# Performance work log

Hardware: AMD Instinct MI355X
Metric: run time of the kernel (lower is better)

## Reference

```python
import jax, jax.numpy as jnp
import numpy as np

DIM = 1536
NH = 24
HD = DIM // NH
EPS = 1e-5


def _ln(x, gamma):
    # LayerNorm over last dim (head_dim), affine weight only, no bias
    mu = jnp.mean(x, axis=-1, keepdims=True)
    var = jnp.var(x, axis=-1, keepdims=True)
    return (x - mu) * jax.lax.rsqrt(var + EPS) * gamma


def setup_inputs() -> dict:
    key = jax.random.key(0)
    ks = jax.random.split(key, 24)
    B, S, T = 1, 2048, 512
    std = 0.02
    d = {
        "hidden_states": jax.random.normal(ks[0], (B, S, DIM), jnp.float32),
        "encoder_hidden_states": jax.random.normal(ks[1], (B, T, DIM), jnp.float32),
        "Wq": jax.random.normal(ks[2], (DIM, DIM), jnp.float32) * std,
        "bq": jnp.zeros((DIM,), jnp.float32),
        "Wk": jax.random.normal(ks[3], (DIM, DIM), jnp.float32) * std,
        "bk": jnp.zeros((DIM,), jnp.float32),
        "Wv": jax.random.normal(ks[4], (DIM, DIM), jnp.float32) * std,
        "bv": jnp.zeros((DIM,), jnp.float32),
        "Waq": jax.random.normal(ks[5], (DIM, DIM), jnp.float32) * std,
        "baq": jnp.zeros((DIM,), jnp.float32),
        "Wak": jax.random.normal(ks[6], (DIM, DIM), jnp.float32) * std,
        "bak": jnp.zeros((DIM,), jnp.float32),
        "Wav": jax.random.normal(ks[7], (DIM, DIM), jnp.float32) * std,
        "bav": jnp.zeros((DIM,), jnp.float32),
        "Wo": jax.random.normal(ks[8], (DIM, DIM), jnp.float32) * std,
        "bo": jnp.zeros((DIM,), jnp.float32),
        "Wao": jax.random.normal(ks[9], (DIM, DIM), jnp.float32) * std,
        "bao": jnp.zeros((DIM,), jnp.float32),
        "gq": jnp.ones((HD,), jnp.float32),
        "gk": jnp.ones((HD,), jnp.float32),
        "gaq": jnp.ones((HD,), jnp.float32),
        "gak": jnp.ones((HD,), jnp.float32),
    }
    return d


def reference(hidden_states, encoder_hidden_states, Wq, bq, Wk, bk, Wv, bv,
              Waq, baq, Wak, bak, Wav, bav, Wo, bo, Wao, bao, gq, gk, gaq, gak):
    B, S, _ = hidden_states.shape
    T = encoder_hidden_states.shape[1]

    def proj(x, W, b):
        # nn.Linear: x @ W.T + b ; reshape to (B, L, NH, HD)
        y = jnp.einsum('bld,ed->ble', x, W) + b
        return y.reshape(B, -1, NH, HD)

    q = _ln(proj(hidden_states, Wq, bq), gq)
    k = _ln(proj(hidden_states, Wk, bk), gk)
    v = proj(hidden_states, Wv, bv)
    eq = _ln(proj(encoder_hidden_states, Waq, baq), gaq)
    ek = _ln(proj(encoder_hidden_states, Wak, bak), gak)
    ev = proj(encoder_hidden_states, Wav, bav)

    q_cat = jnp.concatenate([q, eq], axis=1)  # (B, S+T, H, D)
    k_cat = jnp.concatenate([k, ek], axis=1)
    v_cat = jnp.concatenate([v, ev], axis=1)

    scale = 1.0 / np.sqrt(HD).astype(np.float32)
    scores = jnp.einsum('bqhd,bkhd->bhqk', q_cat, k_cat) * scale
    attn = jax.nn.softmax(scores, axis=-1)
    out = jnp.einsum('bhqk,bkhd->bqhd', attn, v_cat).reshape(B, S + T, DIM)

    img_out = jnp.einsum('bld,ed->ble', out[:, :S], Wo) + bo
    txt_out = jnp.einsum('bld,ed->ble', out[:, S:], Wao) + bao
    return (img_out, txt_out)
```

## Files before the change

### kernel.cpp

```cpp
#include <hip/hip_runtime.h>

#define DIMD 1536
#define LTOT 2560
#define NS 2048
#define NT 512

typedef __bf16 bf16x8 __attribute__((ext_vector_type(8)));
typedef float f32x4 __attribute__((ext_vector_type(4)));
typedef int i32x2 __attribute__((ext_vector_type(2)));
typedef unsigned short u16;
typedef unsigned int u32;

__device__ __forceinline__ u16 f2bf(float f) {
  union { float f; unsigned u; } v; v.f = f;
  return (u16)((v.u + 0x7fffu + ((v.u >> 16) & 1u)) >> 16);
}

__device__ __forceinline__ u32 cvt_pk_bf16(float a, float b) {
  u32 r;
  asm("v_cvt_pk_bf16_f32 %0, %1, %2" : "=v"(r) : "v"(a), "v"(b));
  return r;
}

__device__ __forceinline__ void gload_lds16(const void* g, void* l) {
  __builtin_amdgcn_global_load_lds(
      (__attribute__((address_space(1))) void*)(g),
      (__attribute__((address_space(3))) void*)(l), 16, 0, 0);
}

struct CvtArgs {
  const float* src[10];
  u16* dst[10];
  int n[10];
};

__global__ __launch_bounds__(256) void cvt_all(CvtArgs a) {
  const int seg = blockIdx.y;
  const int n = a.n[seg];
  const float* s = a.src[seg];
  u16* d = a.dst[seg];
  const int i = (blockIdx.x * 256 + threadIdx.x) * 4;
  if (i < n) {
    float4 v = *reinterpret_cast<const float4*>(s + i);
    ushort4 o;
    o.x = f2bf(v.x); o.y = f2bf(v.y); o.z = f2bf(v.z); o.w = f2bf(v.w);
    *reinterpret_cast<ushort4*>(d + i) = o;
  }
}

__device__ __forceinline__ void gemm_mainloop(
    const u16* __restrict__ A, const u16* __restrict__ W,
    u16* As, u16* Bs, f32x4 (&acc)[4][4],
    int w, int lane, int wr, int wc, int l15, int lh) {
  for (int k0 = 0; k0 < DIMD; k0 += 32) {
#pragma unroll
    for (int p = 0; p < 2; ++p) {
      const int c = p * 256 + w * 64 + lane;
      const int row = c >> 2, col = (c & 3) * 8;
      gload_lds16(A + (long)row * DIMD + k0 + col, As + (p * 256 + w * 64) * 8);
      gload_lds16(W + (long)row * DIMD + k0 + col, Bs + (p * 256 + w * 64) * 8);
    }
    __syncthreads();
    bf16x8 af[4], bfr[4];
#pragma unroll
    for (int m = 0; m < 4; ++m)
      af[m] = *reinterpret_cast<const bf16x8*>(As + (wr + m * 16 + l15) * 32 + lh * 8);
#pragma unroll
    for (int n = 0; n < 4; ++n)
      bfr[n] = *reinterpret_cast<const bf16x8*>(Bs + (wc + n * 16 + l15) * 32 + lh * 8);
#pragma unroll
    for (int m = 0; m < 4; ++m)
#pragma unroll
      for (int n = 0; n < 4; ++n)
        acc[m][n] = __builtin_amdgcn_mfma_f32_16x16x32_bf16(af[m], bfr[n], acc[m][n], 0, 0, 0);
    __syncthreads();
  }
}

struct QkvArgs {
  const u16* xb; const u16* exb;
  const u16* w[6];
  const float* b[6];
  const float* g[4];
  u16* qcat; u16* kcat; u16* vcat;
};

__global__ __launch_bounds__(256) void qkv_gemm(QkvArgs a) {
  __shared__ u16 As[128 * 32];
  __shared__ u16 Bs[128 * 32];
  const int tid = threadIdx.x, lane = tid & 63, w = tid >> 6;
  const int l15 = lane & 15, lh = lane >> 4;
  const int side = (blockIdx.x >= 16);
  const int mb = side ? (blockIdx.x - 16) : blockIdx.x;
  const int sel = blockIdx.y / 12;
  const int n0 = (blockIdx.y % 12) * 128;
  const long m0 = (long)mb * 128;
  const long Lbase = side ? NS : 0;
  const int wr = (w >> 1) * 64, wc = (w & 1) * 64;
  const u16* A = (side ? a.exb : a.xb) + m0 * DIMD;
  const u16* W = a.w[side * 3 + sel] + (long)n0 * DIMD;
  const float* bias = a.b[side * 3 + sel];

  f32x4 acc[4][4] = {};
  gemm_mainloop(A, W, As, Bs, acc, w, lane, wr, wc, l15, lh);

  if (sel == 2) {
    u16* out = a.vcat;
#pragma unroll
    for (int m = 0; m < 4; ++m)
#pragma unroll
      for (int r = 0; r < 4; ++r) {
        const long row = Lbase + m0 + wr + m * 16 + lh * 4 + r;
#pragma unroll
        for (int n = 0; n < 4; ++n)
          out[row * DIMD + n0 + wc + n * 16 + l15] =
              f2bf(acc[m][n][r] + bias[n0 + wc + n * 16 + l15]);
      }
  } else {
    const float* gamma = a.g[side * 2 + sel];
    const float gscale = (sel == 0) ? 0.125f * 1.4426950408889634f : 1.0f;
    u16* out = (sel == 0) ? a.qcat : a.kcat;
    const int swz = (sel == 1);
#pragma unroll
    for (int m = 0; m < 4; ++m) {
      float val[4][4];
#pragma unroll
      for (int n = 0; n < 4; ++n) {
        const float b = bias[n0 + wc + n * 16 + l15];
#pragma unroll
        for (int r = 0; r < 4; ++r) val[n][r] = acc[m][n][r] + b;
      }
      float s1[4], s2[4];
#pragma unroll
      for (int r = 0; r < 4; ++r) {
        s1[r] = 0.f; s2[r] = 0.f;
#pragma unroll
        for (int n = 0; n < 4; ++n) { s1[r] += val[n][r]; s2[r] += val[n][r] * val[n][r]; }
      }
#pragma unroll
      for (int off = 1; off < 16; off <<= 1) {
#pragma unroll
        for (int r = 0; r < 4; ++r) {
          s1[r] += __shfl_xor(s1[r], off, 16);
          s2[r] += __shfl_xor(s2[r], off, 16);
        }
      }
#pragma unroll
      for (int r = 0; r < 4; ++r) {
        const float mu = s1[r] * (1.0f / 64.0f);
        const float var = s2[r] * (1.0f / 64.0f) - mu * mu;
        const float rstd = rsqrtf(var + 1e-5f);
        const long row = Lbase + m0 + wr + m * 16 + lh * 4 + r;
        const int r7s = ((lh * 4 + r) & 7) << 3;
#pragma unroll
        for (int n = 0; n < 4; ++n) {
          const float g = gamma[n * 16 + l15] * gscale;
          const int colg = n0 + wc + n * 16 + l15;
          const int colstore = swz ? ((colg & ~63) | ((colg & 63) ^ r7s)) : colg;
          out[row * DIMD + colstore] = f2bf((val[n][r] - mu) * rstd * g);
        }
      }
    }
  }
}

struct OutArgs {
  const u16* aout;
  const u16* w[2];
  const float* b[2];
  float* out;
};

__global__ __launch_bounds__(256) void out_gemm(OutArgs a) {
  __shared__ u16 As[128 * 32];
  __shared__ u16 Bs[128 * 32];
  const int tid = threadIdx.x, lane = tid & 63, w = tid >> 6;
  const int l15 = lane & 15, lh = lane >> 4;
  const int side = (blockIdx.x >= 16);
  const int mb = side ? (blockIdx.x - 16) : blockIdx.x;
  const int n0 = blockIdx.y * 128;
  const long m0 = (long)mb * 128;
  const long Lbase = side ? NS : 0;
  const int wr = (w >> 1) * 64, wc = (w & 1) * 64;
  const u16* A = a.aout + (Lbase + m0) * DIMD;
  const u16* W = a.w[side] + (long)n0 * DIMD;
  const float* bias = a.b[side];

  f32x4 acc[4][4] = {};
  gemm_mainloop(A, W, As, Bs, acc, w, lane, wr, wc, l15, lh);

#pragma unroll
  for (int m = 0; m < 4; ++m)
#pragma unroll
    for (int r = 0; r < 4; ++r) {
      const long row = Lbase + m0 + wr + m * 16 + lh * 4 + r;
#pragma unroll
      for (int n = 0; n < 4; ++n)
        a.out[row * DIMD + n0 + wc + n * 16 + l15] =
            acc[m][n][r] + bias[n0 + wc + n * 16 + l15];
    }
}

__global__ __launch_bounds__(256) void vtrans(const u16* __restrict__ vcat,
                                              u16* __restrict__ VT) {
  const int tid = threadIdx.x;
  const int kv0 = blockIdx.x * 64;
  const int head = blockIdx.y;
  const long hb = (long)head * 64;
#pragma unroll
  for (int p = 0; p < 2; ++p) {
    const int idx = p * 256 + tid;
    const int kl = idx >> 3, db = (idx & 7) * 8;
    uint4 vv = *reinterpret_cast<const uint4*>(vcat + (long)(kv0 + kl) * DIMD + hb + db);
    const u16* vs = reinterpret_cast<const u16*>(&vv);
#pragma unroll
    for (int i = 0; i < 8; ++i) {
      const int d = db + i;
      VT[(hb + d) * LTOT + ((kv0 + kl) ^ ((d & 7) << 3))] = vs[i];
    }
  }
}

__global__ __launch_bounds__(256) void flash_attn(
    const u16* __restrict__ Q, const u16* __restrict__ K,
    const u16* __restrict__ VT, u16* __restrict__ O) {
  __shared__ u16 Ks[128 * 64];
  __shared__ u16 Vs[64 * 128];
  const int tid = threadIdx.x, lane = tid & 63, w = tid >> 6;
  const int l15 = lane & 15, lh = lane >> 4;
  const bool bsel = lh & 1;
  const long hb = (long)blockIdx.y * 64;
  const long q0 = (long)blockIdx.x * 64 + w * 16;
  const int swl = (l15 & 7) << 3;

  bf16x8 aq[2];
#pragma unroll
  for (int kh = 0; kh < 2; ++kh)
    aq[kh] = *reinterpret_cast<const bf16x8*>(Q + (q0 + l15) * DIMD + hb + kh * 32 + lh * 8);

  f32x4 oa[4] = {};
  float lsum = 0.f;

  for (int kv0 = 0; kv0 < LTOT; kv0 += 128) {
#pragma unroll
    for (int ph = 0; ph < 4; ++ph) {
      const int idx = ph * 256 + tid;
      const int rowk = idx >> 3, ck = (idx & 7) * 8;
      gload_lds16(K + (long)(kv0 + rowk) * DIMD + hb + ck, Ks + (ph * 256 + w * 64) * 8);
      const int rowv = idx >> 4, cv = (idx & 15) * 8;
      gload_lds16(VT + (hb + rowv) * LTOT + kv0 + cv, Vs + (ph * 256 + w * 64) * 8);
    }
    __syncthreads();

    f32x4 s[8] = {};
#pragma unroll
    for (int c = 0; c < 8; ++c)
#pragma unroll
      for (int kh = 0; kh < 2; ++kh) {
        bf16x8 kb = *reinterpret_cast<const bf16x8*>(
            Ks + (c * 16 + l15) * 64 + ((kh * 32 + lh * 8) ^ swl));
        s[c] = __builtin_amdgcn_mfma_f32_16x16x32_bf16(kb, aq[kh], s[c], 0, 0, 0);
      }

    u32 lo[8], hi[8];
#pragma unroll
    for (int c = 0; c < 8; ++c) {
      float p0 = exp2f(s[c][0]), p1 = exp2f(s[c][1]);
      float p2 = exp2f(s[c][2]), p3 = exp2f(s[c][3]);
      lsum += (p0 + p1) + (p2 + p3);
      lo[c] = cvt_pk_bf16(p0, p1);
      hi[c] = cvt_pk_bf16(p2, p3);
    }

#pragma unroll
    for (int ks = 0; ks < 4; ++ks) {
      i32x2 L = __builtin_amdgcn_permlane32_swap((int)lo[2 * ks], (int)lo[2 * ks + 1], false, false);
      i32x2 H = __builtin_amdgcn_permlane32_swap((int)hi[2 * ks], (int)hi[2 * ks + 1], false, false);
      const int sLy = __shfl_xor(L.y, 16);
      const int sHy = __shfl_xor(H.y, 16);
      const int sLx = __shfl_xor(L.x, 16);
      const int sHx = __shfl_xor(H.x, 16);
      union { int w4[4]; bf16x8 v; } pu;
      pu.w4[0] = bsel ? sLy : L.x;
      pu.w4[1] = bsel ? sHy : H.x;
      pu.w4[2] = bsel ? L.y : sLx;
      pu.w4[3] = bsel ? H.y : sHx;
#pragma unroll
      for (int dg = 0; dg < 4; ++dg) {
        bf16x8 vb = *reinterpret_cast<const bf16x8*>(
            Vs + (dg * 16 + l15) * 128 + ((ks * 32 + lh * 8) ^ swl));
        oa[dg] = __builtin_amdgcn_mfma_f32_16x16x32_bf16(pu.v, vb, oa[dg], 0, 0, 0);
      }
    }
    __syncthreads();
  }

  lsum += __shfl_xor(lsum, 16);
  lsum += __shfl_xor(lsum, 32);

#pragma unroll
  for (int r = 0; r < 4; ++r) {
    const float inv = 1.0f / __shfl(lsum, lh * 4 + r);
    const long row = q0 + lh * 4 + r;
#pragma unroll
    for (int dg = 0; dg < 4; ++dg)
      O[row * DIMD + hb + dg * 16 + l15] = f2bf(oa[dg][r] * inv);
  }
}

extern "C" void kernel_launch(void* const* d_in, const int* in_sizes, int n_in,
                              void* d_out, int out_size, void* d_ws, size_t ws_size,
                              hipStream_t stream) {
  const float* x   = (const float*)d_in[0];
  const float* ex  = (const float*)d_in[1];
  const float* Wq  = (const float*)d_in[2];  const float* bq  = (const float*)d_in[3];
  const float* Wk  = (const float*)d_in[4];  const float* bk  = (const float*)d_in[5];
  const float* Wv  = (const float*)d_in[6];  const float* bv  = (const float*)d_in[7];
  const float* Waq = (const float*)d_in[8];  const float* baq = (const float*)d_in[9];
  const float* Wak = (const float*)d_in[10]; const float* bak = (const float*)d_in[11];
  const float* Wav = (const float*)d_in[12]; const float* bav = (const float*)d_in[13];
  const float* Wo  = (const float*)d_in[14]; const float* bo  = (const float*)d_in[15];
  const float* Wao = (const float*)d_in[16]; const float* bao = (const float*)d_in[17];
  const float* gq  = (const float*)d_in[18]; const float* gk  = (const float*)d_in[19];
  const float* gaq = (const float*)d_in[20]; const float* gak = (const float*)d_in[21];
  float* out = (float*)d_out;

  u16* ws = (u16*)d_ws;
  const size_t WSZ = (size_t)DIMD * DIMD;
  u16* xb   = ws;
  u16* exb  = xb + (size_t)NS * DIMD;
  u16* wb   = exb + (size_t)NT * DIMD;
  u16* qcat = wb + 8 * WSZ;
  u16* kcat = qcat + (size_t)LTOT * DIMD;
  u16* vcat = kcat + (size_t)LTOT * DIMD;
  u16* VT   = vcat + (size_t)LTOT * DIMD;
  u16* aout = VT + (size_t)LTOT * DIMD;

  CvtArgs ca;
  const float* srcs[10] = {x, ex, Wq, Wk, Wv, Waq, Wak, Wav, Wo, Wao};
  u16* dsts[10] = {xb, exb, wb, wb + WSZ, wb + 2 * WSZ, wb + 3 * WSZ,
                   wb + 4 * WSZ, wb + 5 * WSZ, wb + 6 * WSZ, wb + 7 * WSZ};
  const int ns[10] = {NS * DIMD, NT * DIMD, (int)WSZ, (int)WSZ, (int)WSZ,
                      (int)WSZ, (int)WSZ, (int)WSZ, (int)WSZ, (int)WSZ};
  for (int i = 0; i < 10; ++i) { ca.src[i] = srcs[i]; ca.dst[i] = dsts[i]; ca.n[i] = ns[i]; }
  cvt_all<<<dim3((NS * DIMD) / 1024, 10), 256, 0, stream>>>(ca);

  QkvArgs qa;
  qa.xb = xb; qa.exb = exb;
  qa.w[0] = wb; qa.w[1] = wb + WSZ; qa.w[2] = wb + 2 * WSZ;
  qa.w[3] = wb + 3 * WSZ; qa.w[4] = wb + 4 * WSZ; qa.w[5] = wb + 5 * WSZ;
  qa.b[0] = bq; qa.b[1] = bk; qa.b[2] = bv;
  qa.b[3] = baq; qa.b[4] = bak; qa.b[5] = bav;
  qa.g[0] = gq; qa.g[1] = gk; qa.g[2] = gaq; qa.g[3] = gak;
  qa.qcat = qcat; qa.kcat = kcat; qa.vcat = vcat;
  qkv_gemm<<<dim3(20, 36), 256, 0, stream>>>(qa);

  vtrans<<<dim3(LTOT / 64, 24), 256, 0, stream>>>(vcat, VT);

  flash_attn<<<dim3(LTOT / 64, 24), 256, 0, stream>>>(qcat, kcat, VT, aout);

  OutArgs oa;
  oa.aout = aout;
  oa.w[0] = wb + 6 * WSZ; oa.w[1] = wb + 7 * WSZ;
  oa.b[0] = bo; oa.b[1] = bao;
  oa.out = out;
  out_gemm<<<dim3(20, 12), 256, 0, stream>>>(oa);
}
```

Measured before the change: 368.5 us.

## Double-buffer LDS in GEMM and attention loops, compute row sums via MFMA

```diff
diff --git a/kernel.cpp b/kernel.cpp
--- a/kernel.cpp
+++ b/kernel.cpp
@@ -48,32 +48,58 @@
   }
 }
 
+
+__device__ __forceinline__ void gemm_stage(const u16* pA, const u16* pW,
+                                           u16* As, u16* Bs, int wo) {
+#pragma unroll
+  for (int p = 0; p < 2; ++p) {
+    gload_lds16(pA + (long)p * 64 * DIMD, As + p * 2048 + wo);
+    gload_lds16(pW + (long)p * 64 * DIMD, Bs + p * 2048 + wo);
+  }
+}
+
+__device__ __forceinline__ void gemm_compute(
+    const u16* As, const u16* Bs, f32x4 (&acc)[4][4],
+    int wr, int wc, int l15, int lh) {
+  bf16x8 af[4], bfr[4];
+#pragma unroll
+  for (int m = 0; m < 4; ++m)
+    af[m] = *reinterpret_cast<const bf16x8*>(As + (wr + m * 16 + l15) * 32 + lh * 8);
+#pragma unroll
+  for (int n = 0; n < 4; ++n)
+    bfr[n] = *reinterpret_cast<const bf16x8*>(Bs + (wc + n * 16 + l15) * 32 + lh * 8);
+#pragma unroll
+  for (int m = 0; m < 4; ++m)
+#pragma unroll
+    for (int n = 0; n < 4; ++n)
+      acc[m][n] = __builtin_amdgcn_mfma_f32_16x16x32_bf16(af[m], bfr[n], acc[m][n], 0, 0, 0);
+}
+
 __device__ __forceinline__ void gemm_mainloop(
     const u16* __restrict__ A, const u16* __restrict__ W,
-    u16* As, u16* Bs, f32x4 (&acc)[4][4],
+    u16* As0, u16* Bs0, u16* As1, u16* Bs1, f32x4 (&acc)[4][4],
     int w, int lane, int wr, int wc, int l15, int lh) {
-  for (int k0 = 0; k0 < DIMD; k0 += 32) {
-#pragma unroll
-    for (int p = 0; p < 2; ++p) {
-      const int c = p * 256 + w * 64 + lane;
-      const int row = c >> 2, col = (c & 3) * 8;
-      gload_lds16(A + (long)row * DIMD + k0 + col, As + (p * 256 + w * 64) * 8);
-      gload_lds16(W + (long)row * DIMD + k0 + col, Bs + (p * 256 + w * 64) * 8);
-    }
-    __syncthreads();
-    bf16x8 af[4], bfr[4];
-#pragma unroll
-    for (int m = 0; m < 4; ++m)
-      af[m] = *reinterpret_cast<const bf16x8*>(As + (wr + m * 16 + l15) * 32 + lh * 8);
-#pragma unroll
-    for (int n = 0; n < 4; ++n)
-      bfr[n] = *reinterpret_cast<const bf16x8*>(Bs + (wc + n * 16 + l15) * 32 + lh * 8);
-#pragma unroll
-    for (int m = 0; m < 4; ++m)
-#pragma unroll
-      for (int n = 0; n < 4; ++n)
-        acc[m][n] = __builtin_amdgcn_mfma_f32_16x16x32_bf16(af[m], bfr[n], acc[m][n], 0, 0, 0);
-    __syncthreads();
+  const int base = w * 64 + lane;
+  const u16* pA = A + (long)(base >> 2) * DIMD + (base & 3) * 8;
+  const u16* pW = W + (long)(base >> 2) * DIMD + (base & 3) * 8;
+  const int wo = w * 512;
+
+  gemm_stage(pA, pW, As0, Bs0, wo); pA += 32; pW += 32;
+  for (int k0 = 0; k0 < DIMD; k0 += 64) {
+    gemm_stage(pA, pW, As1, Bs1, wo); pA += 32; pW += 32;
+    asm volatile("s_waitcnt vmcnt(4)" ::: "memory");
+    __builtin_amdgcn_s_barrier();
+    gemm_compute(As0, Bs0, acc, wr, wc, l15, lh);
+    __builtin_amdgcn_s_barrier();
+    if (k0 + 64 < DIMD) {
+      gemm_stage(pA, pW, As0, Bs0, wo); pA += 32; pW += 32;
+      asm volatile("s_waitcnt vmcnt(4)" ::: "memory");
+    } else {
+      asm volatile("s_waitcnt vmcnt(0)" ::: "memory");
+    }
+    __builtin_amdgcn_s_barrier();
+    gemm_compute(As1, Bs1, acc, wr, wc, l15, lh);
+    __builtin_amdgcn_s_barrier();
   }
 }
 
@@ -86,8 +112,10 @@
 };
 
 __global__ __launch_bounds__(256) void qkv_gemm(QkvArgs a) {
-  __shared__ u16 As[128 * 32];
-  __shared__ u16 Bs[128 * 32];
+  __shared__ u16 As0[128 * 32];
+  __shared__ u16 Bs0[128 * 32];
+  __shared__ u16 As1[128 * 32];
+  __shared__ u16 Bs1[128 * 32];
   const int tid = threadIdx.x, lane = tid & 63, w = tid >> 6;
   const int l15 = lane & 15, lh = lane >> 4;
   const int side = (blockIdx.x >= 16);
@@ -102,7 +130,7 @@
   const float* bias = a.b[side * 3 + sel];
 
   f32x4 acc[4][4] = {};
-  gemm_mainloop(A, W, As, Bs, acc, w, lane, wr, wc, l15, lh);
+  gemm_mainloop(A, W, As0, Bs0, As1, Bs1, acc, w, lane, wr, wc, l15, lh);
 
   if (sel == 2) {
     u16* out = a.vcat;
@@ -172,8 +200,10 @@
 };
 
 __global__ __launch_bounds__(256) void out_gemm(OutArgs a) {
-  __shared__ u16 As[128 * 32];
-  __shared__ u16 Bs[128 * 32];
+  __shared__ u16 As0[128 * 32];
+  __shared__ u16 Bs0[128 * 32];
+  __shared__ u16 As1[128 * 32];
+  __shared__ u16 Bs1[128 * 32];
   const int tid = threadIdx.x, lane = tid & 63, w = tid >> 6;
   const int l15 = lane & 15, lh = lane >> 4;
   const int side = (blockIdx.x >= 16);
@@ -187,7 +217,7 @@
   const float* bias = a.b[side];
 
   f32x4 acc[4][4] = {};
-  gemm_mainloop(A, W, As, Bs, acc, w, lane, wr, wc, l15, lh);
+  gemm_mainloop(A, W, As0, Bs0, As1, Bs1, acc, w, lane, wr, wc, l15, lh);
 
 #pragma unroll
   for (int m = 0; m < 4; ++m)
@@ -221,11 +251,66 @@
   }
 }
 
+
+__device__ __forceinline__ void attn_stage(const u16* pK, const u16* pV,
+                                           u16* Ks, u16* Vs, int wo) {
+#pragma unroll
+  for (int ph = 0; ph < 4; ++ph) {
+    gload_lds16(pK + (long)ph * 32 * DIMD, Ks + ph * 2048 + wo);
+    gload_lds16(pV + (long)ph * 16 * LTOT, Vs + ph * 2048 + wo);
+  }
+}
+
+__device__ __forceinline__ void attn_tile(
+    const u16* Ks, const u16* Vs, const bf16x8 (&aq)[2], bf16x8 ones,
+    f32x4 (&oa)[4], f32x4& rs, int l15, int lh, int swl, bool bsel) {
+  f32x4 s[8] = {};
+#pragma unroll
+  for (int c = 0; c < 8; ++c)
+#pragma unroll
+    for (int kh = 0; kh < 2; ++kh) {
+      bf16x8 kb = *reinterpret_cast<const bf16x8*>(
+          Ks + (c * 16 + l15) * 64 + ((kh * 32 + lh * 8) ^ swl));
+      s[c] = __builtin_amdgcn_mfma_f32_16x16x32_bf16(kb, aq[kh], s[c], 0, 0, 0);
+    }
+
+  u32 lo[8], hi[8];
+#pragma unroll
+  for (int c = 0; c < 8; ++c) {
+    lo[c] = cvt_pk_bf16(exp2f(s[c][0]), exp2f(s[c][1]));
+    hi[c] = cvt_pk_bf16(exp2f(s[c][2]), exp2f(s[c][3]));
+  }
+
+#pragma unroll
+  for (int ks = 0; ks < 4; ++ks) {
+    i32x2 L = __builtin_amdgcn_permlane32_swap((int)lo[2 * ks], (int)lo[2 * ks + 1], false, false);
+    i32x2 H = __builtin_amdgcn_permlane32_swap((int)hi[2 * ks], (int)hi[2 * ks + 1], false, false);
+    const int sLy = __shfl_xor(L.y, 16);
+    const int sHy = __shfl_xor(H.y, 16);
+    const int sLx = __shfl_xor(L.x, 16);
+    const int sHx = __shfl_xor(H.x, 16);
+    union { int w4[4]; bf16x8 v; } pu;
+    pu.w4[0] = bsel ? sLy : L.x;
+    pu.w4[1] = bsel ? sHy : H.x;
+    pu.w4[2] = bsel ? L.y : sLx;
+    pu.w4[3] = bsel ? H.y : sHx;
+#pragma unroll
+    for (int dg = 0; dg < 4; ++dg) {
+      bf16x8 vb = *reinterpret_cast<const bf16x8*>(
+          Vs + (dg * 16 + l15) * 128 + ((ks * 32 + lh * 8) ^ swl));
+      oa[dg] = __builtin_amdgcn_mfma_f32_16x16x32_bf16(pu.v, vb, oa[dg], 0, 0, 0);
+    }
+    rs = __builtin_amdgcn_mfma_f32_16x16x32_bf16(pu.v, ones, rs, 0, 0, 0);
+  }
+}
+
 __global__ __launch_bounds__(256) void flash_attn(
     const u16* __restrict__ Q, const u16* __restrict__ K,
     const u16* __restrict__ VT, u16* __restrict__ O) {
-  __shared__ u16 Ks[128 * 64];
-  __shared__ u16 Vs[64 * 128];
+  __shared__ u16 Ks0[128 * 64];
+  __shared__ u16 Vs0[64 * 128];
+  __shared__ u16 Ks1[128 * 64];
+  __shared__ u16 Vs1[64 * 128];
   const int tid = threadIdx.x, lane = tid & 63, w = tid >> 6;
   const int l15 = lane & 15, lh = lane >> 4;
   const bool bsel = lh & 1;
@@ -238,69 +323,38 @@
   for (int kh = 0; kh < 2; ++kh)
     aq[kh] = *reinterpret_cast<const bf16x8*>(Q + (q0 + l15) * DIMD + hb + kh * 32 + lh * 8);
 
+  union { u32 u[4]; bf16x8 v; } onesu;
+#pragma unroll
+  for (int i = 0; i < 4; ++i) onesu.u[i] = 0x3F803F80u;
+
   f32x4 oa[4] = {};
-  float lsum = 0.f;
-
-  for (int kv0 = 0; kv0 < LTOT; kv0 += 128) {
-#pragma unroll
-    for (int ph = 0; ph < 4; ++ph) {
-      const int idx = ph * 256 + tid;
-      const int rowk = idx >> 3, ck = (idx & 7) * 8;
-      gload_lds16(K + (long)(kv0 + rowk) * DIMD + hb + ck, Ks + (ph * 256 + w * 64) * 8);
-      const int rowv = idx >> 4, cv = (idx & 15) * 8;
-      gload_lds16(VT + (hb + rowv) * LTOT + kv0 + cv, Vs + (ph * 256 + w * 64) * 8);
-    }
-    __syncthreads();
-
-    f32x4 s[8] = {};
-#pragma unroll
-    for (int c = 0; c < 8; ++c)
-#pragma unroll
-      for (int kh = 0; kh < 2; ++kh) {
-        bf16x8 kb = *reinterpret_cast<const bf16x8*>(
-            Ks + (c * 16 + l15) * 64 + ((kh * 32 + lh * 8) ^ swl));
-        s[c] = __builtin_amdgcn_mfma_f32_16x16x32_bf16(kb, aq[kh], s[c], 0, 0, 0);
-      }
-
-    u32 lo[8], hi[8];
-#pragma unroll
-    for (int c = 0; c < 8; ++c) {
-      float p0 = exp2f(s[c][0]), p1 = exp2f(s[c][1]);
-      float p2 = exp2f(s[c][2]), p3 = exp2f(s[c][3]);
-      lsum += (p0 + p1) + (p2 + p3);
-      lo[c] = cvt_pk_bf16(p0, p1);
-      hi[c] = cvt_pk_bf16(p2, p3);
-    }
-
-#pragma unroll
-    for (int ks = 0; ks < 4; ++ks) {
-      i32x2 L = __builtin_amdgcn_permlane32_swap((int)lo[2 * ks], (int)lo[2 * ks + 1], false, false);
-      i32x2 H = __builtin_amdgcn_permlane32_swap((int)hi[2 * ks], (int)hi[2 * ks + 1], false, false);
-      const int sLy = __shfl_xor(L.y, 16);
-      const int sHy = __shfl_xor(H.y, 16);
-      const int sLx = __shfl_xor(L.x, 16);
-      const int sHx = __shfl_xor(H.x, 16);
-      union { int w4[4]; bf16x8 v; } pu;
-      pu.w4[0] = bsel ? sLy : L.x;
-      pu.w4[1] = bsel ? sHy : H.x;
-      pu.w4[2] = bsel ? L.y : sLx;
-      pu.w4[3] = bsel ? H.y : sHx;
-#pragma unroll
-      for (int dg = 0; dg < 4; ++dg) {
-        bf16x8 vb = *reinterpret_cast<const bf16x8*>(
-            Vs + (dg * 16 + l15) * 128 + ((ks * 32 + lh * 8) ^ swl));
-        oa[dg] = __builtin_amdgcn_mfma_f32_16x16x32_bf16(pu.v, vb, oa[dg], 0, 0, 0);
-      }
-    }
-    __syncthreads();
-  }
-
-  lsum += __shfl_xor(lsum, 16);
-  lsum += __shfl_xor(lsum, 32);
+  f32x4 rs = {};
+
+  const u16* pK = K + (long)(tid >> 3) * DIMD + hb + (tid & 7) * 8;
+  const u16* pV = VT + (hb + (tid >> 4)) * LTOT + (tid & 15) * 8;
+  const int wo = w * 512;
+
+  attn_stage(pK, pV, Ks0, Vs0, wo); pK += (long)128 * DIMD; pV += 128;
+  for (int kv0 = 0; kv0 < LTOT; kv0 += 256) {
+    attn_stage(pK, pV, Ks1, Vs1, wo); pK += (long)128 * DIMD; pV += 128;
+    asm volatile("s_waitcnt vmcnt(8)" ::: "memory");
+    __builtin_amdgcn_s_barrier();
+    attn_tile(Ks0, Vs0, aq, onesu.v, oa, rs, l15, lh, swl, bsel);
+    __builtin_amdgcn_s_barrier();
+    if (kv0 + 256 < LTOT) {
+      attn_stage(pK, pV, Ks0, Vs0, wo); pK += (long)128 * DIMD; pV += 128;
+      asm volatile("s_waitcnt vmcnt(8)" ::: "memory");
+    } else {
+      asm volatile("s_waitcnt vmcnt(0)" ::: "memory");
+    }
+    __builtin_amdgcn_s_barrier();
+    attn_tile(Ks1, Vs1, aq, onesu.v, oa, rs, l15, lh, swl, bsel);
+    __builtin_amdgcn_s_barrier();
+  }
 
 #pragma unroll
   for (int r = 0; r < 4; ++r) {
-    const float inv = 1.0f / __shfl(lsum, lh * 4 + r);
+    const float inv = 1.0f / rs[r];
     const long row = q0 + lh * 4 + r;
 #pragma unroll
     for (int dg = 0; dg < 4; ++dg)
```

New measurement: 356.7 us. 1.03x faster.
